# Kernel tuning notes

Measured on AMD Instinct MI355X. Metric: run time of the kernel, lower is better.

## Reference

```python
import jax, jax.numpy as jnp
import numpy as np

THRESHOLD = 0.5
NEG_RATIO = 3
ALPHA = 1.0
IMG_SIZE = 300.0  # convert_to_ratio divides pixel coords by image size


def _ssd300_default_boxes():
    """Canonical SSD300 priors: 8732 boxes in (cx, cy, w, h), clipped to [0,1]."""
    fmaps = [38, 19, 10, 5, 3, 1]
    scales = [0.1, 0.2, 0.375, 0.55, 0.725, 0.9]
    ars = [[1.0, 2.0, 0.5],
           [1.0, 2.0, 3.0, 0.5, 1.0 / 3.0],
           [1.0, 2.0, 3.0, 0.5, 1.0 / 3.0],
           [1.0, 2.0, 3.0, 0.5, 1.0 / 3.0],
           [1.0, 2.0, 0.5],
           [1.0, 2.0, 0.5]]
    boxes = []
    for k, (f, s) in enumerate(zip(fmaps, scales)):
        for i in range(f):
            for j in range(f):
                cx = (j + 0.5) / f
                cy = (i + 0.5) / f
                for ar in ars[k]:
                    boxes.append([cx, cy, s * np.sqrt(ar), s / np.sqrt(ar)])
                    if ar == 1.0:
                        s2 = np.sqrt(s * scales[k + 1]) if k < len(fmaps) - 1 else 1.0
                        boxes.append([cx, cy, s2, s2])
    return np.clip(np.asarray(boxes, dtype=np.float32), 0.0, 1.0)  # (8732, 4)


def _cxcy_to_xy(b):
    return jnp.concatenate([b[..., :2] - b[..., 2:] / 2.0,
                            b[..., :2] + b[..., 2:] / 2.0], axis=-1)


def _iou(a, b):
    # a: [N,4] xyxy, b: [P,4] xyxy -> [N,P]
    lt = jnp.maximum(a[:, None, :2], b[None, :, :2])
    rb = jnp.minimum(a[:, None, 2:], b[None, :, 2:])
    wh = jnp.clip(rb - lt, 0.0)
    inter = wh[..., 0] * wh[..., 1]
    area_a = (a[:, 2] - a[:, 0]) * (a[:, 3] - a[:, 1])
    area_b = (b[:, 2] - b[:, 0]) * (b[:, 3] - b[:, 1])
    return inter / (area_a[:, None] + area_b[None, :] - inter)


def _encode_cxcy(t, d):
    # standard SSD offsets (variances 0.1, 0.2). Safe log for unmatched (zero) boxes
    # -- those entries are masked out of the loss, matching torch's positive-only gather.
    g_cxcy = (t[..., :2] - d[..., :2]) / (d[..., 2:] / 10.0)
    safe_wh = jnp.where(t[..., 2:] > 0.0, t[..., 2:], d[..., 2:])
    g_wh = jnp.log(safe_wh / d[..., 2:]) * 5.0
    return jnp.concatenate([g_cxcy, g_wh], axis=-1)


def setup_inputs() -> dict:
    key = jax.random.key(0)
    k1, k2, k3, k4 = jax.random.split(key, 4)
    B, P, C, N = 128, 8732, 81, 16
    predicted_boxes = jax.random.normal(k1, (B, P, 4), dtype=jnp.float32)
    predicted_scores = jax.random.normal(k2, (B, P, C), dtype=jnp.float32)
    u = jax.random.uniform(k3, (B, N, 4), dtype=jnp.float32)
    cxcy = (0.15 + 0.7 * u[..., :2]) * IMG_SIZE   # centers in pixel coords
    wh = (0.08 + 0.32 * u[..., 2:]) * IMG_SIZE    # sizes in pixel coords
    target_boxes = jnp.concatenate([cxcy, wh], axis=-1)
    target_labels = jax.random.randint(k4, (B, N), 1, C)
    default_boxes = jnp.asarray(_ssd300_default_boxes())
    return {"predicted_boxes": predicted_boxes,
            "predicted_scores": predicted_scores,
            "target_boxes": target_boxes,
            "target_labels": target_labels,
            "default_boxes": default_boxes}


def reference(predicted_boxes, predicted_scores, target_boxes, target_labels, default_boxes):
    B, P, C = predicted_scores.shape
    db_xy = _cxcy_to_xy(default_boxes)
    tb = target_boxes / IMG_SIZE  # convert_to_ratio

    def match(boxes, labels):
        # boxes: [N,4] cxcywh (ratio), labels: [N]
        ov = _iou(_cxcy_to_xy(boxes), db_xy)          # [N, P]
        best_ov = ov.max(axis=0)                      # [P]
        obj_idx = ov.argmax(axis=0)                   # [P]
        box_idx = ov.argmax(axis=1)                   # [N] best prior per object
        obj_idx = obj_idx.at[box_idx].set(jnp.arange(boxes.shape[0]))
        check = best_ov > THRESHOLD                   # uses pre-scatter max (faithful)
        t_lab = jnp.where(check, labels[obj_idx], 0)
        t_box = jnp.where(check[:, None], boxes[obj_idx], 0.0)
        return _encode_cxcy(t_box, default_boxes), t_lab

    true_bboxes, true_labels = jax.vmap(match)(tb, target_labels)  # [B,P,4], [B,P]

    positive = true_labels != 0                        # [B,P]
    n_pos = jnp.maximum(positive.sum(), 1)

    # SmoothL1 (beta=1), mean over positive elements (num_pos * 4)
    diff = jnp.abs(predicted_boxes - true_bboxes)
    sl1 = jnp.where(diff < 1.0, 0.5 * diff * diff, diff - 0.5)
    bbox_loss = (sl1 * positive[..., None]).sum() / (n_pos.astype(sl1.dtype) * 4.0)

    # per-box cross entropy
    logp = jax.nn.log_softmax(predicted_scores, axis=-1)
    cls_all = -jnp.take_along_axis(logp, true_labels[..., None], axis=-1)[..., 0]  # [B,P]

    cls_pos_sum = (cls_all * positive).sum()
    neg = jnp.where(positive, 0.0, cls_all)
    neg_sorted = -jnp.sort(-neg, axis=1)               # descending per image
    n_hard = positive.sum(axis=1) * NEG_RATIO          # [B]
    rank = jnp.arange(P)[None, :]
    hard_neg_sum = (neg_sorted * (rank < n_hard[:, None])).sum()

    cls_loss = (cls_pos_sum + hard_neg_sum) / n_pos.astype(cls_all.dtype)
    return cls_loss + ALPHA * bbox_loss
```

## Files before the change

kernel.cpp:

```cpp
#include <hip/hip_runtime.h>
#include <hip/hip_bf16.h>
#include <math.h>

#define BB 128
#define PP 8732
#define NN 16
#define CC 81
#define IMG 300.0f
#define TILE_ROWS 64
#define NT ((BB * PP) / TILE_ROWS)
#define K1_THREADS 512

__global__ __launch_bounds__(K1_THREADS) void k1_match(
    const float* __restrict__ pred_boxes,
    const float* __restrict__ tgt_boxes,
    const int*   __restrict__ tgt_labels,
    const float* __restrict__ dboxes,
    int*   __restrict__ tlab_out,
    float* __restrict__ bbox_partial,
    int*   __restrict__ pos_count,
    int*   __restrict__ k3_done)
{
    const int b   = blockIdx.x;
    const int tid = threadIdx.x;
    const int NW  = K1_THREADS / 64;

    if (b == 0 && tid == 0) *k3_done = 0;

    __shared__ float t_cx[NN], t_cy[NN], t_w[NN], t_h[NN];
    __shared__ float t_x0s[NN], t_y0s[NN], t_x1s[NN], t_y1s[NN], t_areas[NN];
    __shared__ int   t_lab[NN];
    __shared__ unsigned short obj_s[PP];
    __shared__ unsigned char  chk_s[PP];
    __shared__ float red_iv[NN][NW];
    __shared__ float red_dv[NN][NW];
    __shared__ int   red_pv[NN][NW];
    __shared__ int   box_idx_s[NN];
    __shared__ float red_f[NW];
    __shared__ int   red_c[NW];

    if (tid < NN) {
        const float* tb = tgt_boxes + ((size_t)b * NN + tid) * 4;
        float cx = tb[0] / IMG, cy = tb[1] / IMG, w = tb[2] / IMG, h = tb[3] / IMG;
        t_cx[tid] = cx; t_cy[tid] = cy; t_w[tid] = w; t_h[tid] = h;
        float x0 = cx - w * 0.5f, y0 = cy - h * 0.5f;
        float x1 = cx + w * 0.5f, y1 = cy + h * 0.5f;
        t_x0s[tid] = x0; t_y0s[tid] = y0; t_x1s[tid] = x1; t_y1s[tid] = y1;
        t_areas[tid] = (x1 - x0) * (y1 - y0);
        t_lab[tid] = tgt_labels[(size_t)b * NN + tid];
    }
    __syncthreads();

    float tx0[NN], ty0[NN], tx1[NN], ty1[NN], tar[NN];
#pragma unroll
    for (int n = 0; n < NN; ++n) {
        tx0[n] = t_x0s[n]; ty0[n] = t_y0s[n];
        tx1[n] = t_x1s[n]; ty1[n] = t_y1s[n];
        tar[n] = t_areas[n];
    }

    float besti[NN], bestd[NN];
    int   bestp[NN];
#pragma unroll
    for (int n = 0; n < NN; ++n) { besti[n] = 0.0f; bestd[n] = 1.0f; bestp[n] = 0x7fffffff; }

    for (int p = tid; p < PP; p += K1_THREADS) {
        float4 d = *reinterpret_cast<const float4*>(dboxes + (size_t)p * 4);
        float dx0 = d.x - d.z * 0.5f, dy0 = d.y - d.w * 0.5f;
        float dx1 = d.x + d.z * 0.5f, dy1 = d.y + d.w * 0.5f;
        float dar = (dx1 - dx0) * (dy1 - dy0);
        float bi = 0.0f, bd = 1.0f; int bidx = 0;
#pragma unroll
        for (int n = 0; n < NN; ++n) {
            float lx = fmaxf(tx0[n], dx0);
            float ly = fmaxf(ty0[n], dy0);
            float rx = fminf(tx1[n], dx1);
            float ry = fminf(ty1[n], dy1);
            float iw = fmaxf(rx - lx, 0.0f);
            float ih = fmaxf(ry - ly, 0.0f);
            float inter = iw * ih;
            float den   = tar[n] + dar - inter;
            if (inter * bd > bi * den) { bi = inter; bd = den; bidx = n; }
            if (inter * bestd[n] > besti[n] * den || bestp[n] == 0x7fffffff) {
                besti[n] = inter; bestd[n] = den; bestp[n] = p;
            }
        }
        obj_s[p] = (unsigned short)bidx;
        chk_s[p] = (bi > 0.5f * bd) ? 1 : 0;
    }

#pragma unroll
    for (int n = 0; n < NN; ++n) {
        float vi = besti[n], vd = bestd[n]; int vp = bestp[n];
        for (int off = 32; off; off >>= 1) {
            float i2 = __shfl_xor(vi, off);
            float d2 = __shfl_xor(vd, off);
            int   p2 = __shfl_xor(vp, off);
            float a = i2 * vd, q = vi * d2;
            if (a > q || (a == q && p2 < vp)) { vi = i2; vd = d2; vp = p2; }
        }
        if ((tid & 63) == 0) {
            red_iv[n][tid >> 6] = vi; red_dv[n][tid >> 6] = vd; red_pv[n][tid >> 6] = vp;
        }
    }
    __syncthreads();
    if (tid < NN) {
        float vi = red_iv[tid][0], vd = red_dv[tid][0]; int vp = red_pv[tid][0];
        for (int w = 1; w < NW; ++w) {
            float i2 = red_iv[tid][w], d2 = red_dv[tid][w]; int p2 = red_pv[tid][w];
            float a = i2 * vd, q = vi * d2;
            if (a > q || (a == q && p2 < vp)) { vi = i2; vd = d2; vp = p2; }
        }
        box_idx_s[tid] = vp;
    }
    __syncthreads();
    if (tid == 0) {
        for (int n = 0; n < NN; ++n) obj_s[box_idx_s[n]] = (unsigned short)n;
    }
    __syncthreads();

    float bacc = 0.0f;
    int   pcnt = 0;
    for (int p = tid; p < PP; p += K1_THREADS) {
        int lab = 0;
        if (chk_s[p]) {
            int n = obj_s[p];
            lab = t_lab[n];
            if (lab != 0) {
                ++pcnt;
                float4 d = *reinterpret_cast<const float4*>(dboxes + (size_t)p * 4);
                float gx = (t_cx[n] - d.x) / (d.z / 10.0f);
                float gy = (t_cy[n] - d.y) / (d.w / 10.0f);
                float gw = logf(t_w[n] / d.z) * 5.0f;
                float gh = logf(t_h[n] / d.w) * 5.0f;
                float4 pv = *reinterpret_cast<const float4*>(pred_boxes + ((size_t)b * PP + p) * 4);
                float dfs[4] = { pv.x - gx, pv.y - gy, pv.z - gw, pv.w - gh };
#pragma unroll
                for (int j = 0; j < 4; ++j) {
                    float ad = fabsf(dfs[j]);
                    bacc += (ad < 1.0f) ? 0.5f * ad * ad : ad - 0.5f;
                }
            }
        }
        tlab_out[(size_t)b * PP + p] = lab;
    }
    for (int off = 32; off; off >>= 1) {
        bacc += __shfl_xor(bacc, off);
        pcnt += __shfl_xor(pcnt, off);
    }
    if ((tid & 63) == 0) { red_f[tid >> 6] = bacc; red_c[tid >> 6] = pcnt; }
    __syncthreads();
    if (tid == 0) {
        float s = 0.0f; int c = 0;
        for (int w = 0; w < NW; ++w) { s += red_f[w]; c += red_c[w]; }
        bbox_partial[b] = s;
        pos_count[b]    = c;
    }
}

__global__ __launch_bounds__(256) void k2_cls(
    const float* __restrict__ scores,
    const int*   __restrict__ tlab,
    float* __restrict__ neg,
    float* __restrict__ clspos_partial)
{
    __shared__ float slds[TILE_ROWS * CC];
    const int tid = threadIdx.x;
    const int t   = blockIdx.x;

    const float* g = scores + (size_t)t * (TILE_ROWS * CC);
    for (int i = tid; i < TILE_ROWS * CC; i += 256)
        slds[i] = g[i];
    __syncthreads();

    const int row = tid >> 2;
    const int q   = tid & 3;
    const float* myrow = &slds[row * CC];
    const int base = q * 20;

    float x[21];
#pragma unroll
    for (int i = 0; i < 20; ++i) x[i] = myrow[base + i];
    x[20] = (q == 3) ? myrow[80] : -1e30f;

    float m = x[0];
#pragma unroll
    for (int i = 1; i < 21; ++i) m = fmaxf(m, x[i]);
    m = fmaxf(m, __shfl_xor(m, 1));
    m = fmaxf(m, __shfl_xor(m, 2));

    float s0 = 0.0f, s1 = 0.0f, s2 = 0.0f, s3 = 0.0f;
#pragma unroll
    for (int i = 0; i < 20; i += 4) {
        s0 += __expf(x[i + 0] - m);
        s1 += __expf(x[i + 1] - m);
        s2 += __expf(x[i + 2] - m);
        s3 += __expf(x[i + 3] - m);
    }
    s0 += __expf(x[20] - m);
    float s = (s0 + s1) + (s2 + s3);
    s += __shfl_xor(s, 1);
    s += __shfl_xor(s, 2);

    float acc = 0.0f;
    if (q == 0) {
        long long r = (long long)t * TILE_ROWS + row;
        int   lab = tlab[r];
        float cls = m + __logf(s) - slds[row * CC + lab];
        if (lab != 0) { acc = cls; neg[r] = 0.0f; }
        else          { neg[r] = cls; }
    }

    for (int off = 32; off; off >>= 1) acc += __shfl_xor(acc, off);
    __shared__ float wsum[4];
    if ((tid & 63) == 0) wsum[tid >> 6] = acc;
    __syncthreads();
    if (tid == 0)
        clspos_partial[t] = wsum[0] + wsum[1] + wsum[2] + wsum[3];
}

#define HREP 32
#define HPAD 257
#define CH   ((NT + BB - 1) / BB)
__global__ __launch_bounds__(256) void k3_topk_final(
    const float* __restrict__ neg,
    const int*   __restrict__ pos_count,
    const float* __restrict__ clspos_partial,
    const float* __restrict__ bbox_partial,
    float* __restrict__ hard_partial,
    float* __restrict__ clspos_red,
    int*   __restrict__ done,
    float* __restrict__ out)
{
    const int b   = blockIdx.x;
    const int tid = threadIdx.x;
    const int rep = (tid & 63) >> 1;
    const int wv  = tid >> 6;

    __shared__ unsigned int vals[PP];
    __shared__ int histR[HREP * HPAD];
    __shared__ int scn[256];
    __shared__ unsigned int s_prefix;
    __shared__ int s_kk;
    __shared__ float wsum[4];
    __shared__ float wsumc[4];
    __shared__ int s_last;

    for (int i = tid; i < PP; i += 256)
        vals[i] = __float_as_uint(neg[(size_t)b * PP + i]);

    {
        int start = b * CH;
        int end   = start + CH; if (end > NT) end = NT;
        float cv = (start + tid < end) ? clspos_partial[start + tid] : 0.0f;
        for (int off = 32; off; off >>= 1) cv += __shfl_xor(cv, off);
        if ((tid & 63) == 0) wsumc[wv] = cv;
    }

    int k = pos_count[b] * 3;
    if (k > PP) k = PP;
    if (tid == 0) { s_prefix = 0u; s_kk = k; }
    __syncthreads();
    if (tid == 0)
        clspos_red[b] = wsumc[0] + wsumc[1] + wsumc[2] + wsumc[3];

    float hp = 0.0f;
    if (k > 0) {
        unsigned int prefmask = 0u;
        for (int round = 0; round < 4; ++round) {
            const int shift = 24 - 8 * round;
            for (int i = tid; i < HREP * HPAD; i += 256) histR[i] = 0;
            __syncthreads();
            unsigned int pref = s_prefix;
            for (int i = tid; i < PP; i += 256) {
                unsigned int v = vals[i];
                if ((v & prefmask) == pref)
                    atomicAdd(&histR[rep * HPAD + ((v >> shift) & 0xFF)], 1);
            }
            __syncthreads();
            int myh = 0;
#pragma unroll 8
            for (int r = 0; r < HREP; ++r) myh += histR[r * HPAD + tid];
            scn[tid] = myh;
            __syncthreads();
            for (int off = 1; off < 256; off <<= 1) {
                int add = (tid + off < 256) ? scn[tid + off] : 0;
                __syncthreads();
                scn[tid] += add;
                __syncthreads();
            }
            int sg = scn[tid] - myh;
            int kk = s_kk;
            __syncthreads();
            if (sg < kk && sg + myh >= kk) {
                s_prefix = pref | ((unsigned int)tid << shift);
                s_kk     = kk - sg;
            }
            __syncthreads();
            prefmask |= (0xFFu << shift);
        }

        unsigned int t = s_prefix;
        int kk = s_kk;
        float tf = __uint_as_float(t);

        float acc = 0.0f;
        for (int i = tid; i < PP; i += 256) {
            unsigned int v = vals[i];
            if (v > t) acc += __uint_as_float(v);
        }
        for (int off = 32; off; off >>= 1) acc += __shfl_xor(acc, off);
        if ((tid & 63) == 0) wsum[tid >> 6] = acc;
        __syncthreads();
        if (tid == 0)
            hp = wsum[0] + wsum[1] + wsum[2] + wsum[3] + (float)kk * tf;
    }
    if (tid == 0) hard_partial[b] = hp;

    __threadfence();
    if (tid == 0) s_last = (atomicAdd(done, 1) == BB - 1) ? 1 : 0;
    __syncthreads();
    if (!s_last) return;
    __threadfence();

    float cacc = 0.0f, bacc = 0.0f, hacc = 0.0f;
    int   pacc = 0;
    if (tid < BB) {
        cacc = clspos_red[tid];
        bacc = bbox_partial[tid];
        hacc = hard_partial[tid];
        pacc = pos_count[tid];
    }
    __shared__ float sc[256], sb[256], sh[256];
    __shared__ int   sp[256];
    sc[tid] = cacc; sb[tid] = bacc; sh[tid] = hacc; sp[tid] = pacc;
    __syncthreads();
    for (int off = 128; off; off >>= 1) {
        if (tid < off) {
            sc[tid] += sc[tid + off];
            sb[tid] += sb[tid + off];
            sh[tid] += sh[tid + off];
            sp[tid] += sp[tid + off];
        }
        __syncthreads();
    }
    if (tid == 0) {
        float npos = fmaxf((float)sp[0], 1.0f);
        out[0] = (sc[0] + sh[0]) / npos + sb[0] / (npos * 4.0f);
    }
}

extern "C" void kernel_launch(void* const* d_in, const int* in_sizes, int n_in,
                              void* d_out, int out_size, void* d_ws, size_t ws_size,
                              hipStream_t stream) {
    const float* pred_boxes  = (const float*)d_in[0];
    const float* pred_scores = (const float*)d_in[1];
    const float* tgt_boxes   = (const float*)d_in[2];
    const int*   tgt_labels  = (const int*)d_in[3];
    const float* dboxes      = (const float*)d_in[4];
    float* out = (float*)d_out;

    char* ws = (char*)d_ws;
    int*   tlab           = (int*)ws;   ws += (size_t)BB * PP * sizeof(int);
    float* neg            = (float*)ws; ws += (size_t)BB * PP * sizeof(float);
    int*   pos_count      = (int*)ws;   ws += BB * sizeof(int);
    float* bbox_partial   = (float*)ws; ws += BB * sizeof(float);
    float* hard_partial   = (float*)ws; ws += BB * sizeof(float);
    float* clspos_red     = (float*)ws; ws += BB * sizeof(float);
    int*   k3_done        = (int*)ws;   ws += 4 * sizeof(int);
    float* clspos_partial = (float*)ws; ws += (size_t)NT * sizeof(float);

    k1_match<<<BB, K1_THREADS, 0, stream>>>(pred_boxes, tgt_boxes, tgt_labels, dboxes,
                                            tlab, bbox_partial, pos_count, k3_done);
    k2_cls<<<NT, 256, 0, stream>>>(pred_scores, tlab, neg, clspos_partial);
    k3_topk_final<<<BB, 256, 0, stream>>>(neg, pos_count, clspos_partial,
                                          bbox_partial, hard_partial, clspos_red,
                                          k3_done, out);
}
```

Measured before the change: 146.3 us.

## Widen top-k block to 1024 threads and use wave-shuffle scans in radix select

```diff
diff --git a/kernel.cpp b/kernel.cpp
--- a/kernel.cpp
+++ b/kernel.cpp
@@ -10,6 +10,7 @@
 #define TILE_ROWS 64
 #define NT ((BB * PP) / TILE_ROWS)
 #define K1_THREADS 512
+#define K3_THREADS 1024
 
 __global__ __launch_bounds__(K1_THREADS) void k1_match(
     const float* __restrict__ pred_boxes,
@@ -222,7 +223,7 @@
 #define HREP 32
 #define HPAD 257
 #define CH   ((NT + BB - 1) / BB)
-__global__ __launch_bounds__(256) void k3_topk_final(
+__global__ __launch_bounds__(K3_THREADS) void k3_topk_final(
     const float* __restrict__ neg,
     const int*   __restrict__ pos_count,
     const float* __restrict__ clspos_partial,
@@ -232,88 +233,106 @@
     int*   __restrict__ done,
     float* __restrict__ out)
 {
-    const int b   = blockIdx.x;
-    const int tid = threadIdx.x;
-    const int rep = (tid & 63) >> 1;
-    const int wv  = tid >> 6;
+    const int b    = blockIdx.x;
+    const int tid  = threadIdx.x;
+    const int lane = tid & 63;
+    const int wv   = tid >> 6;
+    const int rep  = lane >> 1;
 
     __shared__ unsigned int vals[PP];
     __shared__ int histR[HREP * HPAD];
     __shared__ int scn[256];
+    __shared__ int waveTot[4];
     __shared__ unsigned int s_prefix;
     __shared__ int s_kk;
-    __shared__ float wsum[4];
-    __shared__ float wsumc[4];
+    __shared__ float wsum[16];
+    __shared__ float wsumc[16];
     __shared__ int s_last;
-
-    for (int i = tid; i < PP; i += 256)
-        vals[i] = __float_as_uint(neg[(size_t)b * PP + i]);
+    __shared__ float fin[4][2];
+
+    {
+        const uint4* src = reinterpret_cast<const uint4*>(neg + (size_t)b * PP);
+        uint4* dst = reinterpret_cast<uint4*>(vals);
+        for (int i = tid; i < PP / 4; i += K3_THREADS) dst[i] = src[i];
+    }
 
     {
         int start = b * CH;
         int end   = start + CH; if (end > NT) end = NT;
-        float cv = (start + tid < end) ? clspos_partial[start + tid] : 0.0f;
+        float cv = (start + tid < end && tid < CH) ? clspos_partial[start + tid] : 0.0f;
         for (int off = 32; off; off >>= 1) cv += __shfl_xor(cv, off);
-        if ((tid & 63) == 0) wsumc[wv] = cv;
+        if (lane == 0) wsumc[wv] = cv;
     }
 
     int k = pos_count[b] * 3;
     if (k > PP) k = PP;
     if (tid == 0) { s_prefix = 0u; s_kk = k; }
     __syncthreads();
-    if (tid == 0)
-        clspos_red[b] = wsumc[0] + wsumc[1] + wsumc[2] + wsumc[3];
+    if (tid == 0) {
+        float c = 0.0f;
+        for (int w = 0; w < 16; ++w) c += wsumc[w];
+        clspos_red[b] = c;
+    }
 
     float hp = 0.0f;
     if (k > 0) {
         unsigned int prefmask = 0u;
         for (int round = 0; round < 4; ++round) {
             const int shift = 24 - 8 * round;
-            for (int i = tid; i < HREP * HPAD; i += 256) histR[i] = 0;
+            for (int i = tid; i < HREP * HPAD; i += K3_THREADS) histR[i] = 0;
             __syncthreads();
-            unsigned int pref = s_prefix;
-            for (int i = tid; i < PP; i += 256) {
+            const unsigned int pref = s_prefix;
+            const int kkR = s_kk;
+            for (int i = tid; i < PP; i += K3_THREADS) {
                 unsigned int v = vals[i];
                 if ((v & prefmask) == pref)
                     atomicAdd(&histR[rep * HPAD + ((v >> shift) & 0xFF)], 1);
             }
             __syncthreads();
-            int myh = 0;
+            int myh = 0, s = 0;
+            if (tid < 256) {
 #pragma unroll 8
-            for (int r = 0; r < HREP; ++r) myh += histR[r * HPAD + tid];
-            scn[tid] = myh;
+                for (int r = 0; r < HREP; ++r) myh += histR[r * HPAD + tid];
+                s = myh;
+#pragma unroll
+                for (int off = 1; off < 64; off <<= 1) {
+                    int v = __shfl_down(s, off);
+                    if (lane + off < 64) s += v;
+                }
+                if (lane == 0) waveTot[wv] = s;
+            }
             __syncthreads();
-            for (int off = 1; off < 256; off <<= 1) {
-                int add = (tid + off < 256) ? scn[tid + off] : 0;
-                __syncthreads();
-                scn[tid] += add;
-                __syncthreads();
-            }
-            int sg = scn[tid] - myh;
-            int kk = s_kk;
-            __syncthreads();
-            if (sg < kk && sg + myh >= kk) {
-                s_prefix = pref | ((unsigned int)tid << shift);
-                s_kk     = kk - sg;
+            if (tid < 256) {
+                int addhi = 0;
+                for (int w2 = wv + 1; w2 < 4; ++w2) addhi += waveTot[w2];
+                s += addhi;
+                int sg = s - myh;
+                if (sg < kkR && sg + myh >= kkR) {
+                    s_prefix = pref | ((unsigned int)tid << shift);
+                    s_kk     = kkR - sg;
+                }
             }
             __syncthreads();
             prefmask |= (0xFFu << shift);
         }
 
-        unsigned int t = s_prefix;
-        int kk = s_kk;
-        float tf = __uint_as_float(t);
+        const unsigned int t = s_prefix;
+        const int kk = s_kk;
+        const float tf = __uint_as_float(t);
 
         float acc = 0.0f;
-        for (int i = tid; i < PP; i += 256) {
+        for (int i = tid; i < PP; i += K3_THREADS) {
             unsigned int v = vals[i];
             if (v > t) acc += __uint_as_float(v);
         }
         for (int off = 32; off; off >>= 1) acc += __shfl_xor(acc, off);
-        if ((tid & 63) == 0) wsum[tid >> 6] = acc;
+        if (lane == 0) wsum[wv] = acc;
         __syncthreads();
-        if (tid == 0)
-            hp = wsum[0] + wsum[1] + wsum[2] + wsum[3] + (float)kk * tf;
+        if (tid == 0) {
+            float ssum = 0.0f;
+            for (int w = 0; w < 16; ++w) ssum += wsum[w];
+            hp = ssum + (float)kk * tf;
+        }
     }
     if (tid == 0) hard_partial[b] = hp;
 
@@ -323,30 +342,30 @@
     if (!s_last) return;
     __threadfence();
 
-    float cacc = 0.0f, bacc = 0.0f, hacc = 0.0f;
-    int   pacc = 0;
+    float cacc = 0.0f, bacc = 0.0f, hacc = 0.0f, pacc = 0.0f;
     if (tid < BB) {
         cacc = clspos_red[tid];
         bacc = bbox_partial[tid];
         hacc = hard_partial[tid];
-        pacc = pos_count[tid];
-    }
-    __shared__ float sc[256], sb[256], sh[256];
-    __shared__ int   sp[256];
-    sc[tid] = cacc; sb[tid] = bacc; sh[tid] = hacc; sp[tid] = pacc;
-    __syncthreads();
-    for (int off = 128; off; off >>= 1) {
-        if (tid < off) {
-            sc[tid] += sc[tid + off];
-            sb[tid] += sb[tid + off];
-            sh[tid] += sh[tid + off];
-            sp[tid] += sp[tid + off];
-        }
-        __syncthreads();
-    }
+        pacc = (float)pos_count[tid];
+    }
+    for (int off = 32; off; off >>= 1) {
+        cacc += __shfl_xor(cacc, off);
+        bacc += __shfl_xor(bacc, off);
+        hacc += __shfl_xor(hacc, off);
+        pacc += __shfl_xor(pacc, off);
+    }
+    if (lane == 0 && wv < 2) {
+        fin[0][wv] = cacc; fin[1][wv] = bacc; fin[2][wv] = hacc; fin[3][wv] = pacc;
+    }
+    __syncthreads();
     if (tid == 0) {
-        float npos = fmaxf((float)sp[0], 1.0f);
-        out[0] = (sc[0] + sh[0]) / npos + sb[0] / (npos * 4.0f);
+        float c = fin[0][0] + fin[0][1];
+        float bx = fin[1][0] + fin[1][1];
+        float h = fin[2][0] + fin[2][1];
+        float np = fin[3][0] + fin[3][1];
+        float npos = fmaxf(np, 1.0f);
+        out[0] = (c + h) / npos + bx / (npos * 4.0f);
     }
 }
 
@@ -373,7 +392,7 @@
     k1_match<<<BB, K1_THREADS, 0, stream>>>(pred_boxes, tgt_boxes, tgt_labels, dboxes,
                                             tlab, bbox_partial, pos_count, k3_done);
     k2_cls<<<NT, 256, 0, stream>>>(pred_scores, tlab, neg, clspos_partial);
-    k3_topk_final<<<BB, 256, 0, stream>>>(neg, pos_count, clspos_partial,
-                                          bbox_partial, hard_partial, clspos_red,
-                                          k3_done, out);
+    k3_topk_final<<<BB, K3_THREADS, 0, stream>>>(neg, pos_count, clspos_partial,
+                                                 bbox_partial, hard_partial, clspos_red,
+                                                 k3_done, out);
 }
```

After: 162.2 us. +10.9%, slower.
